# Performance work log

Hardware: AMD Instinct MI355X
Metric: run time of the kernel (lower is better)

The kernel has to match this reference:

```python
import jax, jax.numpy as jnp
import numpy as np

B, T, H, D, NC, M = 2, 8192, 8, 64, 128, 4
COMMITMENT = 1e-4
EPS_NORM = 1e-6
EPS_SCATTER = 1e-5


def setup_inputs() -> dict:
    key = jax.random.key(0)
    ks = jax.random.split(key, 6)
    dm = H * D
    return {
        "q": jax.random.normal(ks[0], (B, T, dm), jnp.float32),
        "k": jax.random.normal(ks[1], (B, T, dm), jnp.float32),
        "v": jax.random.normal(ks[2], (B, T, dm), jnp.float32),
        "means": jax.random.normal(ks[3], (H, NC, D), jnp.float32),
        "mem_key": jax.random.normal(ks[4], (H, NC, M, D), jnp.float32),
        "mem_value": jax.random.normal(ks[5], (H, NC, M, D), jnp.float32),
    }


def _safe_normalize(x):
    return x / (jnp.linalg.norm(x, axis=-1, keepdims=True) + EPS_NORM)


def _cdist(x, means):
    # x: (b,h,T,d), means: (h,nc,d) -> (b,h,T,nc) euclidean distances
    x2 = jnp.sum(x * x, axis=-1, keepdims=True)          # (b,h,T,1)
    m2 = jnp.sum(means * means, axis=-1)                 # (h,nc)
    xm = jnp.einsum('bhtd,hcd->bhtc', x, means)          # (b,h,T,nc)
    return jnp.sqrt(jnp.maximum(x2 + m2[None, :, None, :] - 2.0 * xm, 0.0))


def _distribution(dists, w):
    # dists: (b,h,T,nc). Select the w nearest tokens per cluster.
    neg = -jnp.swapaxes(dists, -1, -2)                   # (b,h,nc,T)
    _, idx = jax.lax.top_k(neg, w)                       # (b,h,nc,w)
    b, h, nc, _ = idx.shape
    return idx.reshape(b, h, nc * w)


def _scatter_mean(vals, indices, t):
    # vals: (b,h,n,d), indices: (b,h,n) -> (b,h,t,d) mean-combined
    b, h, n, d = vals.shape
    offs = (jnp.arange(b * h, dtype=indices.dtype) * t).reshape(b, h, 1)
    flat = (indices + offs).reshape(-1)
    numer = jax.ops.segment_sum(vals.reshape(-1, d), flat, num_segments=b * h * t)
    denom = jax.ops.segment_sum(jnp.ones((b * h * n,), vals.dtype), flat, num_segments=b * h * t)
    return (numer / (denom[:, None] + EPS_SCATTER)).reshape(b, h, t, d)


def reference(q, k, v, means, mem_key, mem_value):
    b, t, dm = q.shape
    h, d, nc = H, D, NC
    # torch uses q.view(b, h, t, d): a pure reinterpretation, i.e. reshape.
    q = q.reshape(b, h, t, d)
    k = k.reshape(b, h, t, d)
    v = v.reshape(b, h, t, d)

    # --- kmeans routing (indices are non-differentiable, matching torch.no_grad) ---
    x = jnp.concatenate([q, k], axis=2)                  # (b,h,2t,d)
    xn = _safe_normalize(x)
    dists = _cdist(xn, means)                            # (b,h,2t,nc)
    buckets = jnp.argmin(dists, axis=-1)                 # (b,h,2t)
    routed = means[jnp.arange(h)[None, :, None], buckets]  # (b,h,2t,d)
    aux_loss = jnp.mean((xn - routed) ** 2) * COMMITMENT

    w = t // nc
    q_dists, k_dists = dists[:, :, :t], dists[:, :, t:]
    indices = _distribution(q_dists, w)                  # (b,h,nc*w)
    kv_indices = _distribution(k_dists, w)               # (b,h,nc*w)

    # --- gather into clusters ---
    qc = jnp.take_along_axis(q, indices[..., None], axis=2).reshape(b, h, nc, w, d)
    kc = jnp.take_along_axis(k, kv_indices[..., None], axis=2).reshape(b, h, nc, w, d)
    vc = jnp.take_along_axis(v, kv_indices[..., None], axis=2).reshape(b, h, nc, w, d)

    # --- mem kv concat ---
    mk = jnp.broadcast_to(mem_key[None], (b,) + mem_key.shape)
    mv = jnp.broadcast_to(mem_value[None], (b,) + mem_value.shape)
    kf = jnp.concatenate([mk, kc], axis=3)               # (b,h,nc,M+w,d)
    vf = jnp.concatenate([mv, vc], axis=3)

    # --- blocked attention per cluster ---
    dots = jnp.einsum('bhnid,bhnjd->bhnij', qc, kf) * (d ** -0.5)
    attn = jax.nn.softmax(dots, axis=-1)
    out = jnp.einsum('bhnij,bhnjd->bhnid', attn, vf).reshape(b, h, nc * w, d)

    # --- scatter_mean combine back to sequence order ---
    return _scatter_mean(out, indices, t), aux_loss
```

## Files before the change

### kernel.cpp

```cpp
#include <hip/hip_runtime.h>
#include <math.h>

#define BB 2
#define TT 8192
#define HH 8
#define DD 64
#define NCC 128
#define MM 4
#define WW (TT/NCC)
#define T2 (2*TT)
#define SMAX 32
#define SK 65
#define TIEMAX 256

__global__ __launch_bounds__(256) void kdist(
    const float* __restrict__ q, const float* __restrict__ k,
    const float* __restrict__ means,
    float* __restrict__ qd, float* __restrict__ kd, float* __restrict__ aux)
{
  __shared__ float sm[NCC * DD];
  __shared__ float sm2[NCC];
  __shared__ float red[4];
  const int b = blockIdx.z, h = blockIdx.y;
  const int tid = threadIdx.x;

  const float4* mp = (const float4*)(means + (size_t)h * NCC * DD);
  float4* smp = (float4*)sm;
  for (int i = tid; i < NCC * DD / 4; i += 256) smp[i] = mp[i];
  __syncthreads();
  if (tid < NCC) {
    float s = 0.f;
    #pragma unroll
    for (int d = 0; d < DD; ++d) { float v = sm[tid * DD + d]; s += v * v; }
    sm2[tid] = s;
  }
  __syncthreads();

  const int tp = blockIdx.x * 256 + tid;
  const size_t bh = (size_t)(b * HH + h);
  const float* src = (tp < TT) ? (q + (bh * TT + tp) * DD)
                               : (k + (bh * TT + (tp - TT)) * DD);
  float x[DD];
  float ss = 0.f;
  #pragma unroll
  for (int i = 0; i < DD / 4; ++i) {
    float4 v = ((const float4*)src)[i];
    x[4*i] = v.x; x[4*i+1] = v.y; x[4*i+2] = v.z; x[4*i+3] = v.w;
    ss += v.x*v.x + v.y*v.y + v.z*v.z + v.w*v.w;
  }
  const float scale = 1.f / (sqrtf(ss) + 1e-6f);
  float x2 = 0.f;
  #pragma unroll
  for (int i = 0; i < DD; ++i) { x[i] *= scale; x2 += x[i] * x[i]; }

  float* dst = (tp < TT) ? (qd + (bh * NCC) * TT + tp)
                         : (kd + (bh * NCC) * TT + (tp - TT));
  float mind2 = 1e30f;
  for (int c = 0; c < NCC; ++c) {
    const float* mrow = sm + c * DD;
    float dot = 0.f;
    #pragma unroll
    for (int d = 0; d < DD; ++d) dot += x[d] * mrow[d];
    float d2 = fmaxf(x2 + sm2[c] - 2.f * dot, 0.f);
    mind2 = fminf(mind2, d2);
    dst[(size_t)c * TT] = sqrtf(d2);
  }

  float v = mind2;
  #pragma unroll
  for (int off = 32; off; off >>= 1) v += __shfl_down(v, off, 64);
  if ((tid & 63) == 0) red[tid >> 6] = v;
  __syncthreads();
  if (tid == 0) atomicAdd(aux, red[0] + red[1] + red[2] + red[3]);
}

__global__ __launch_bounds__(256) void ktopk(
    const float* __restrict__ qd, const float* __restrict__ kd,
    int* __restrict__ idxq, int* __restrict__ idxk)
{
  __shared__ unsigned int red[4];
  __shared__ int outIdx[WW];
  __shared__ int tie[TIEMAX];
  __shared__ int pos, tpos;

  const int c = blockIdx.x, h = blockIdx.y;
  const int b = blockIdx.z >> 1, isK = blockIdx.z & 1;
  const int tid = threadIdx.x;
  const int lane = tid & 63, wid = tid >> 6;
  const size_t rowoff = ((size_t)(b * HH + h) * NCC + c) * TT;
  const float4* row4 = (const float4*)((isK ? kd : qd) + rowoff);

  unsigned int u[32];
  #pragma unroll
  for (int j = 0; j < 8; ++j) {
    float4 v = row4[j * 256 + tid];
    u[4*j+0] = __float_as_uint(v.x);
    u[4*j+1] = __float_as_uint(v.y);
    u[4*j+2] = __float_as_uint(v.z);
    u[4*j+3] = __float_as_uint(v.w);
  }
  if (tid == 0) { pos = 0; tpos = 0; }

  unsigned int tau = 0u;
  for (int bit = 30; bit >= 0; --bit) {
    const unsigned int cand = tau | (1u << bit);
    int cnt = 0;
    #pragma unroll
    for (int i = 0; i < 32; ++i) cnt += (u[i] < cand) ? 1 : 0;
    #pragma unroll
    for (int off = 32; off; off >>= 1) cnt += __shfl_down(cnt, off, 64);
    if (lane == 0) red[wid] = (unsigned int)cnt;
    __syncthreads();
    const int tot = (int)(red[0] + red[1] + red[2] + red[3]);
    if (tot < WW) tau = cand;
    __syncthreads();
  }
  {
    int cnt = 0;
    #pragma unroll
    for (int i = 0; i < 32; ++i) cnt += (u[i] < tau) ? 1 : 0;
    #pragma unroll
    for (int off = 32; off; off >>= 1) cnt += __shfl_down(cnt, off, 64);
    if (lane == 0) red[wid] = (unsigned int)cnt;
  }
  __syncthreads();
  const int base = (int)(red[0] + red[1] + red[2] + red[3]);
  const int need = WW - base;

  #pragma unroll
  for (int i = 0; i < 32; ++i) {
    const int idx = (i >> 2) * 1024 + tid * 4 + (i & 3);
    if (u[i] < tau) {
      int p = atomicAdd(&pos, 1); outIdx[p] = idx;
    } else if (u[i] == tau) {
      int p = atomicAdd(&tpos, 1);
      if (p < TIEMAX) tie[p] = idx;
    }
  }
  __syncthreads();
  const int tc = tpos < TIEMAX ? tpos : TIEMAX;
  if (tc == need) {
    if (tid < need) outIdx[base + tid] = tie[tid];
  } else if (tid == 0) {
    int last = -1;
    for (int e = 0; e < need; ++e) {
      int mn = 0x7fffffff;
      for (int s = 0; s < tc; ++s) { int t = tie[s]; if (t > last && t < mn) mn = t; }
      outIdx[base + e] = mn; last = mn;
    }
  }
  __syncthreads();
  int* dstp = (isK ? idxk : idxq) + ((size_t)(b * HH + h) * NCC + c) * WW;
  if (tid < WW) dstp[tid] = outIdx[tid];
}

__global__ __launch_bounds__(256) void kattn(
    const float* __restrict__ q, const float* __restrict__ kg,
    const float* __restrict__ vg, const float* __restrict__ memk,
    const float* __restrict__ memv, const int* __restrict__ idxq,
    const int* __restrict__ idxk, float* __restrict__ outc)
{
  __shared__ float Ks[(MM + WW) * SK];
  __shared__ float Vs[(MM + WW) * SK];
  __shared__ int tq[WW];
  __shared__ int tk[WW];

  const int c = blockIdx.x, h = blockIdx.y, b = blockIdx.z;
  const int tid = threadIdx.x;
  const size_t bh = (size_t)(b * HH + h);

  if (tid < WW) tq[tid] = idxq[(bh * NCC + c) * WW + tid];
  else if (tid < 2 * WW) tk[tid - WW] = idxk[(bh * NCC + c) * WW + tid - WW];
  __syncthreads();

  const int r = tid >> 2, part = tid & 3;

  for (int j = r; j < MM + WW; j += 64) {
    const float* sk = (j < MM)
        ? memk + (((size_t)(h * NCC + c)) * MM + j) * DD + part * 16
        : kg + (bh * TT + tk[j - MM]) * DD + part * 16;
    const float* sv = (j < MM)
        ? memv + (((size_t)(h * NCC + c)) * MM + j) * DD + part * 16
        : vg + (bh * TT + tk[j - MM]) * DD + part * 16;
    #pragma unroll
    for (int i = 0; i < 4; ++i) {
      *(float4*)&Ks[j * SK + part * 16 + 4 * i] = ((const float4*)sk)[i];
      *(float4*)&Vs[j * SK + part * 16 + 4 * i] = ((const float4*)sv)[i];
    }
  }
  __syncthreads();

  float s[17];
  {
    float qr[DD];
    const float* qsrc = q + (bh * TT + tq[r]) * DD;
    #pragma unroll
    for (int i = 0; i < DD / 4; ++i) {
      float4 v = ((const float4*)qsrc)[i];
      qr[4*i] = v.x; qr[4*i+1] = v.y; qr[4*i+2] = v.z; qr[4*i+3] = v.w;
    }
    #pragma unroll
    for (int jj = 0; jj < 17; ++jj) {
      const float* krow = &Ks[(part * 17 + jj) * SK];
      float acc = 0.f;
      #pragma unroll
      for (int d = 0; d < DD; ++d) acc += qr[d] * krow[d];
      s[jj] = acc * 0.125f;
    }
  }
  float mx = s[0];
  #pragma unroll
  for (int jj = 1; jj < 17; ++jj) mx = fmaxf(mx, s[jj]);
  mx = fmaxf(mx, __shfl_xor(mx, 1, 64));
  mx = fmaxf(mx, __shfl_xor(mx, 2, 64));
  float sum = 0.f;
  #pragma unroll
  for (int jj = 0; jj < 17; ++jj) { s[jj] = expf(s[jj] - mx); sum += s[jj]; }
  sum += __shfl_xor(sum, 1, 64);
  sum += __shfl_xor(sum, 2, 64);
  const float inv = 1.f / sum;
  #pragma unroll
  for (int jj = 0; jj < 17; ++jj) s[jj] *= inv;

  float acc[DD];
  #pragma unroll
  for (int d = 0; d < DD; ++d) acc[d] = 0.f;
  #pragma unroll
  for (int jj = 0; jj < 17; ++jj) {
    const float p = s[jj];
    const float* vrow = &Vs[(part * 17 + jj) * SK];
    #pragma unroll
    for (int d = 0; d < DD; ++d) acc[d] += p * vrow[d];
  }
  #pragma unroll
  for (int d = 0; d < DD; ++d) {
    acc[d] += __shfl_xor(acc[d], 1, 64);
    acc[d] += __shfl_xor(acc[d], 2, 64);
  }
  float* obase = outc + (((bh * NCC + c) * WW) + r) * DD + part * 16;
  #pragma unroll
  for (int i = 0; i < 4; ++i)
    ((float4*)obase)[i] = make_float4(acc[part*16+4*i], acc[part*16+4*i+1],
                                      acc[part*16+4*i+2], acc[part*16+4*i+3]);
}

__global__ __launch_bounds__(256) void kindex(
    const int* __restrict__ idxq, const float* __restrict__ outc,
    int* __restrict__ cnt, int* __restrict__ slots, float* __restrict__ out)
{
  const int i = blockIdx.x * 256 + threadIdx.x;
  const int bh = i >> 13;
  const int e = i & 8191;
  const int t = idxq[i];
  const int row = bh * TT + t;
  const int p = atomicAdd(&cnt[row], 1);
  if (p < SMAX) {
    slots[(size_t)row * SMAX + p] = e;
  } else {
    const float* src = outc + ((size_t)(bh * (NCC * WW)) + e) * DD;
    for (int d = 0; d < DD; ++d) atomicAdd(&out[(size_t)row * DD + d], src[d]);
  }
}

__global__ __launch_bounds__(256) void kfinal(
    float* __restrict__ outp, const int* __restrict__ cnt,
    const int* __restrict__ slots, const float* __restrict__ outc,
    const float* __restrict__ aux)
{
  const size_t n = (size_t)BB * HH * TT * DD;
  const size_t i = (size_t)blockIdx.x * 256 + threadIdx.x;
  if (i < n) {
    const int row = (int)(i >> 6);
    const int d = (int)(i & 63);
    const int bh = row >> 13;
    const int c = cnt[row];
    const int m = c < SMAX ? c : SMAX;
    float sum = outp[i];
    for (int s = 0; s < m; ++s) {
      const int e = slots[(size_t)row * SMAX + s];
      sum += outc[((size_t)(bh * (NCC * WW)) + e) * DD + d];
    }
    outp[i] = sum / ((float)c + 1e-5f);
  }
  if (i == 0) outp[n] = aux[0] * (0.0001f / (float)((size_t)BB * HH * 2 * TT * DD));
}

extern "C" void kernel_launch(void* const* d_in, const int* in_sizes, int n_in,
                              void* d_out, int out_size, void* d_ws, size_t ws_size,
                              hipStream_t stream) {
  (void)in_sizes; (void)n_in; (void)out_size; (void)ws_size;
  const float* q     = (const float*)d_in[0];
  const float* k     = (const float*)d_in[1];
  const float* v     = (const float*)d_in[2];
  const float* means = (const float*)d_in[3];
  const float* memk  = (const float*)d_in[4];
  const float* memv  = (const float*)d_in[5];
  float* out = (float*)d_out;

  const size_t NQ   = (size_t)BB * HH * NCC * TT;
  const size_t NIDX = (size_t)BB * HH * NCC * WW;
  const size_t NROW = (size_t)BB * HH * TT;

  float* qd   = (float*)d_ws;
  float* kd   = qd + NQ;
  int*   idxq = (int*)(kd + NQ);
  int*   idxk = idxq + NIDX;
  int*   cnt  = idxk + NIDX;
  float* aux  = (float*)(cnt + NROW);
  float* outc  = qd;
  int*   slots = (int*)kd;

  const size_t n = (size_t)BB * HH * TT * DD;
  hipMemsetAsync(out, 0, n * sizeof(float), stream);
  hipMemsetAsync(cnt, 0, (NROW + 1) * sizeof(int), stream);

  kdist<<<dim3(T2 / 256, HH, BB), 256, 0, stream>>>(q, k, means, qd, kd, aux);
  ktopk<<<dim3(NCC, HH, 2 * BB), 256, 0, stream>>>(qd, kd, idxq, idxk);
  kattn<<<dim3(NCC, HH, BB), 256, 0, stream>>>(q, k, v, memk, memv, idxq, idxk, outc);
  kindex<<<(int)(NIDX / 256), 256, 0, stream>>>(idxq, outc, cnt, slots, out);
  kfinal<<<(int)((n + 255) / 256), 256, 0, stream>>>(out, cnt, slots, outc, aux);
}
```

Measured before the change: 478.0 us.

## Split kdist over centroid halves and restructure attention PV with shared probabilities

The distance kernel now splits the 128 centroids into two 64-centroid halves across blocks. This doubles the grid and halves the shared memory footprint. Per-token minimum distances are combined with atomicMin into a new buffer, and a separate kaux kernel sums them. In the attention kernel, QK dot products use float4 LDS reads with four accumulators, and SK is padded to 68 for alignment. The PV stage writes softmax probabilities to shared memory so each thread accumulates only its 16-wide slice over all keys, which removes the 64-register accumulator and the shuffle reductions. The cost is an extra memset and launch, plus extra syncs.

```diff
diff --git a/kernel.cpp b/kernel.cpp
--- a/kernel.cpp
+++ b/kernel.cpp
@@ -9,26 +9,28 @@
 #define MM 4
 #define WW (TT/NCC)
 #define T2 (2*TT)
+#define CH 64
 #define SMAX 32
-#define SK 65
+#define SK 68
 #define TIEMAX 256
 
 __global__ __launch_bounds__(256) void kdist(
     const float* __restrict__ q, const float* __restrict__ k,
     const float* __restrict__ means,
-    float* __restrict__ qd, float* __restrict__ kd, float* __restrict__ aux)
-{
-  __shared__ float sm[NCC * DD];
-  __shared__ float sm2[NCC];
-  __shared__ float red[4];
-  const int b = blockIdx.z, h = blockIdx.y;
+    float* __restrict__ qd, float* __restrict__ kd,
+    unsigned int* __restrict__ minb)
+{
+  __shared__ float sm[CH * DD];
+  __shared__ float sm2[CH];
+  const int b = blockIdx.z >> 1, h = blockIdx.y;
+  const int c0 = (blockIdx.z & 1) * CH;
   const int tid = threadIdx.x;
 
-  const float4* mp = (const float4*)(means + (size_t)h * NCC * DD);
+  const float4* mp = (const float4*)(means + ((size_t)h * NCC + c0) * DD);
   float4* smp = (float4*)sm;
-  for (int i = tid; i < NCC * DD / 4; i += 256) smp[i] = mp[i];
-  __syncthreads();
-  if (tid < NCC) {
+  for (int i = tid; i < CH * DD / 4; i += 256) smp[i] = mp[i];
+  __syncthreads();
+  if (tid < CH) {
     float s = 0.f;
     #pragma unroll
     for (int d = 0; d < DD; ++d) { float v = sm[tid * DD + d]; s += v * v; }
@@ -56,22 +58,30 @@
   float* dst = (tp < TT) ? (qd + (bh * NCC) * TT + tp)
                          : (kd + (bh * NCC) * TT + (tp - TT));
   float mind2 = 1e30f;
-  for (int c = 0; c < NCC; ++c) {
+  for (int c = 0; c < CH; ++c) {
     const float* mrow = sm + c * DD;
     float dot = 0.f;
     #pragma unroll
     for (int d = 0; d < DD; ++d) dot += x[d] * mrow[d];
     float d2 = fmaxf(x2 + sm2[c] - 2.f * dot, 0.f);
     mind2 = fminf(mind2, d2);
-    dst[(size_t)c * TT] = sqrtf(d2);
-  }
-
-  float v = mind2;
+    dst[(size_t)(c0 + c) * TT] = sqrtf(d2);
+  }
+
+  atomicMin(&minb[bh * T2 + tp], __float_as_uint(mind2));
+}
+
+__global__ __launch_bounds__(256) void kaux(
+    const unsigned int* __restrict__ minb, float* __restrict__ aux)
+{
+  __shared__ float red[4];
+  const int i = blockIdx.x * 256 + threadIdx.x;
+  float v = __uint_as_float(minb[i]);
   #pragma unroll
   for (int off = 32; off; off >>= 1) v += __shfl_down(v, off, 64);
-  if ((tid & 63) == 0) red[tid >> 6] = v;
-  __syncthreads();
-  if (tid == 0) atomicAdd(aux, red[0] + red[1] + red[2] + red[3]);
+  if ((threadIdx.x & 63) == 0) red[threadIdx.x >> 6] = v;
+  __syncthreads();
+  if (threadIdx.x == 0) atomicAdd(aux, red[0] + red[1] + red[2] + red[3]);
 }
 
 __global__ __launch_bounds__(256) void ktopk(
@@ -201,11 +211,17 @@
     }
     #pragma unroll
     for (int jj = 0; jj < 17; ++jj) {
-      const float* krow = &Ks[(part * 17 + jj) * SK];
-      float acc = 0.f;
+      const float4* krow = (const float4*)&Ks[(part * 17 + jj) * SK];
+      float a0 = 0.f, a1 = 0.f, a2 = 0.f, a3 = 0.f;
       #pragma unroll
-      for (int d = 0; d < DD; ++d) acc += qr[d] * krow[d];
-      s[jj] = acc * 0.125f;
+      for (int i = 0; i < DD / 4; ++i) {
+        float4 kv = krow[i];
+        a0 = fmaf(qr[4*i+0], kv.x, a0);
+        a1 = fmaf(qr[4*i+1], kv.y, a1);
+        a2 = fmaf(qr[4*i+2], kv.z, a2);
+        a3 = fmaf(qr[4*i+3], kv.w, a3);
+      }
+      s[jj] = ((a0 + a1) + (a2 + a3)) * 0.125f;
     }
   }
   float mx = s[0];
@@ -222,26 +238,27 @@
   #pragma unroll
   for (int jj = 0; jj < 17; ++jj) s[jj] *= inv;
 
-  float acc[DD];
-  #pragma unroll
-  for (int d = 0; d < DD; ++d) acc[d] = 0.f;
-  #pragma unroll
-  for (int jj = 0; jj < 17; ++jj) {
-    const float p = s[jj];
-    const float* vrow = &Vs[(part * 17 + jj) * SK];
-    #pragma unroll
-    for (int d = 0; d < DD; ++d) acc[d] += p * vrow[d];
-  }
-  #pragma unroll
-  for (int d = 0; d < DD; ++d) {
-    acc[d] += __shfl_xor(acc[d], 1, 64);
-    acc[d] += __shfl_xor(acc[d], 2, 64);
-  }
-  float* obase = outc + (((bh * NCC + c) * WW) + r) * DD + part * 16;
-  #pragma unroll
-  for (int i = 0; i < 4; ++i)
-    ((float4*)obase)[i] = make_float4(acc[part*16+4*i], acc[part*16+4*i+1],
-                                      acc[part*16+4*i+2], acc[part*16+4*i+3]);
+  __syncthreads();
+  #pragma unroll
+  for (int jj = 0; jj < 17; ++jj) Ks[r * SK + part * 17 + jj] = s[jj];
+  __syncthreads();
+
+  float4 a0 = make_float4(0.f,0.f,0.f,0.f), a1 = a0, a2 = a0, a3 = a0;
+  for (int j = 0; j < MM + WW; ++j) {
+    const float p = Ks[r * SK + j];
+    const float4* vrow = (const float4*)&Vs[j * SK + part * 16];
+    float4 v0 = vrow[0], v1 = vrow[1], v2 = vrow[2], v3 = vrow[3];
+    a0.x = fmaf(p, v0.x, a0.x); a0.y = fmaf(p, v0.y, a0.y);
+    a0.z = fmaf(p, v0.z, a0.z); a0.w = fmaf(p, v0.w, a0.w);
+    a1.x = fmaf(p, v1.x, a1.x); a1.y = fmaf(p, v1.y, a1.y);
+    a1.z = fmaf(p, v1.z, a1.z); a1.w = fmaf(p, v1.w, a1.w);
+    a2.x = fmaf(p, v2.x, a2.x); a2.y = fmaf(p, v2.y, a2.y);
+    a2.z = fmaf(p, v2.z, a2.z); a2.w = fmaf(p, v2.w, a2.w);
+    a3.x = fmaf(p, v3.x, a3.x); a3.y = fmaf(p, v3.y, a3.y);
+    a3.z = fmaf(p, v3.z, a3.z); a3.w = fmaf(p, v3.w, a3.w);
+  }
+  float4* obase = (float4*)(outc + (((bh * NCC + c) * WW) + r) * DD + part * 16);
+  obase[0] = a0; obase[1] = a1; obase[2] = a2; obase[3] = a3;
 }
 
 __global__ __launch_bounds__(256) void kindex(
@@ -300,21 +317,25 @@
   const size_t NQ   = (size_t)BB * HH * NCC * TT;
   const size_t NIDX = (size_t)BB * HH * NCC * WW;
   const size_t NROW = (size_t)BB * HH * TT;
-
-  float* qd   = (float*)d_ws;
-  float* kd   = qd + NQ;
-  int*   idxq = (int*)(kd + NQ);
-  int*   idxk = idxq + NIDX;
-  int*   cnt  = idxk + NIDX;
-  float* aux  = (float*)(cnt + NROW);
-  float* outc  = qd;
-  int*   slots = (int*)kd;
+  const size_t NMIN = (size_t)BB * HH * T2;
+
+  float*        qd   = (float*)d_ws;
+  float*        kd   = qd + NQ;
+  int*          idxq = (int*)(kd + NQ);
+  int*          idxk = idxq + NIDX;
+  int*          cnt  = idxk + NIDX;
+  float*        aux  = (float*)(cnt + NROW);
+  unsigned int* minb = (unsigned int*)(aux + 1);
+  float*        outc  = qd;
+  int*          slots = (int*)kd;
 
   const size_t n = (size_t)BB * HH * TT * DD;
   hipMemsetAsync(out, 0, n * sizeof(float), stream);
   hipMemsetAsync(cnt, 0, (NROW + 1) * sizeof(int), stream);
-
-  kdist<<<dim3(T2 / 256, HH, BB), 256, 0, stream>>>(q, k, means, qd, kd, aux);
+  hipMemsetAsync(minb, 0x7f, NMIN * sizeof(unsigned int), stream);
+
+  kdist<<<dim3(T2 / 256, HH, BB * 2), 256, 0, stream>>>(q, k, means, qd, kd, minb);
+  kaux<<<(int)(NMIN / 256), 256, 0, stream>>>(minb, aux);
   ktopk<<<dim3(NCC, HH, 2 * BB), 256, 0, stream>>>(qd, kd, idxq, idxk);
   kattn<<<dim3(NCC, HH, BB), 256, 0, stream>>>(q, k, v, memk, memv, idxq, idxk, outc);
   kindex<<<(int)(NIDX / 256), 256, 0, stream>>>(idxq, outc, cnt, slots, out);
```

After: 429.2 us. 10.2% less time.
